# Kernel optimization log

Hardware: AMD Instinct MI355X
Metric: run time of the kernel (lower is better)

Reference implementation:

```python
import jax, jax.numpy as jnp
import numpy as np

N, H, B = 500000, 256, 512  # nodes, hidden_dim, number of graphs


def setup_inputs() -> dict:
    key = jax.random.key(0)
    k1, k2, k3, k4 = jax.random.split(key, 4)
    x = jax.random.normal(k1, (N, H), dtype=jnp.float32)
    batch = jnp.sort(jax.random.randint(k2, (N,), 0, B)).astype(jnp.int64)
    # attention_pool params (Linear(H,H) -> Tanh -> Linear(H,1))
    s1 = 1.0 / np.sqrt(H)
    W1 = jax.random.uniform(k3, (H, H), jnp.float32, -s1, s1)
    b1 = jnp.zeros((H,), jnp.float32)
    W2 = jax.random.uniform(k4, (H, 1), jnp.float32, -s1, s1)
    b2 = jnp.zeros((1,), jnp.float32)
    return {"x": x, "batch": batch, "W1": W1, "b1": b1, "W2": W2, "b2": b2}


def reference(x, batch, W1, b1, W2, b2):
    # attention scores per node: Linear -> tanh -> Linear -> scalar
    s = (jnp.tanh(x @ W1 + b1) @ W2 + b2)[:, 0]            # [N]
    # segment-wise softmax over nodes of each graph (numerically stable)
    seg_max = jax.ops.segment_max(s, batch, num_segments=B)  # [B]
    e = jnp.exp(s - seg_max[batch])                          # [N]
    denom = jax.ops.segment_sum(e, batch, num_segments=B)    # [B]
    w = e / denom[batch]                                     # [N]
    attn_pool = jax.ops.segment_sum(x * w[:, None], batch, num_segments=B)  # [B,H]
    # mean pool
    sums = jax.ops.segment_sum(x, batch, num_segments=B)     # [B,H]
    counts = jax.ops.segment_sum(jnp.ones((x.shape[0],), x.dtype), batch, num_segments=B)
    mean_pool = sums / jnp.maximum(counts, 1.0)[:, None]
    # max pool (guard empty segments -> 0, matching zero-init buffer behavior)
    max_pool = jax.ops.segment_max(x, batch, num_segments=B)
    max_pool = jnp.where(counts[:, None] > 0, max_pool, 0.0)
    return jnp.concatenate([mean_pool, max_pool, attn_pool], axis=1)  # [B, 3H]
```

## Files before the change

kernel.cpp:

```cpp
#include <hip/hip_runtime.h>

#define HDIM 256
#define MTILE 64
#define NITER 4
#define APITCH 264

typedef __attribute__((ext_vector_type(8))) short short8;
typedef __attribute__((ext_vector_type(4))) short short4v;
typedef __attribute__((ext_vector_type(4))) float floatx4;

__device__ __forceinline__ unsigned short f2bf(float f){
  unsigned u = __float_as_uint(f);
  u += 0x7FFFu + ((u>>16)&1u);
  return (unsigned short)(u>>16);
}
__device__ __forceinline__ unsigned fkey(float f){
  unsigned u = __float_as_uint(f);
  return u ^ ((unsigned)((int)u>>31) | 0x80000000u);
}
__device__ __forceinline__ float fdec(unsigned u){
  unsigned b = (u & 0x80000000u) ? (u & 0x7FFFFFFFu) : ~u;
  return __uint_as_float(b);
}

__global__ void k_pre(const float* __restrict__ W1, unsigned short* __restrict__ W1T,
                      const int* __restrict__ batch, int* __restrict__ segstart,
                      float* __restrict__ zbuf, int zerowords, int n, int B,
                      int ZB, int PB){
  const int bid = blockIdx.x, t = threadIdx.x;
  if (bid < ZB){
    int i = bid*256 + t;
    if (i < zerowords) zbuf[i] = 0.f;
  } else if (bid < ZB + PB){
    int col = bid - ZB;
    W1T[col*HDIM + t] = f2bf(W1[t*HDIM + col]);
  } else {
    int i = (bid - ZB - PB)*256 + t;
    if (i >= n) return;
    int b = batch[i];
    int prev = (i == 0) ? -1 : batch[i-1];
    if (prev != b) for (int q = prev+1; q <= b; ++q) segstart[q] = i;
    if (i == n-1) for (int q = b+1; q <= B; ++q) segstart[q] = n;
  }
}

__launch_bounds__(256)
__global__ void k_main(const float* __restrict__ x,
                       const unsigned short* __restrict__ w1t,
                       const float* __restrict__ b1,
                       const float* __restrict__ w2,
                       const float* __restrict__ b2,
                       const int* __restrict__ batch,
                       float* __restrict__ denom,
                       float* __restrict__ sums,
                       unsigned* __restrict__ maxu,
                       float* __restrict__ attn,
                       int n)
{
  __shared__ unsigned short As[MTILE*APITCH];
  __shared__ float sp[4][MTILE];
  __shared__ float earr[MTILE];
  __shared__ int sbat[MTILE*NITER];
  const int t = threadIdx.x;
  const int wv = t>>6;
  const int lane = t&63;
  const int l15 = lane&15;
  const int quad = lane>>4;
  const long long base = (long long)blockIdx.x * (MTILE*NITER);

  { long long gr = base + t; sbat[t] = (gr < n) ? batch[gr] : -1; }

  short8 bf[8][4];
  float b1v[4], w2v[4];
  const int cb = wv*64;
  #pragma unroll
  for (int ct=0; ct<4; ++ct){
    int col = cb + ct*16 + l15;
    b1v[ct] = b1[col];
    w2v[ct] = w2[col];
    #pragma unroll
    for (int kc=0; kc<8; ++kc)
      bf[kc][ct] = *(const short8*)(w1t + (size_t)col*HDIM + kc*32 + quad*8);
  }
  const float b2v = b2[0];

  float psum = 0.f, patt = 0.f, pmx = -INFINITY;
  int curb = -1;

  const float4* x4 = (const float4*)x;
  for (int it = 0; it < NITER; ++it){
    const long long node0 = base + (long long)it*MTILE;
    if (node0 >= n) break;

    #pragma unroll
    for (int j=0; j<MTILE/4; ++j){
      int f = j*256 + t;
      int row = f>>6, c4 = f&63;
      long long gr = node0 + row;
      float4 v = make_float4(0.f,0.f,0.f,0.f);
      if (gr < n) v = x4[gr*(HDIM/4) + c4];
      short4v p;
      p.x=(short)f2bf(v.x); p.y=(short)f2bf(v.y); p.z=(short)f2bf(v.z); p.w=(short)f2bf(v.w);
      *(short4v*)(As + row*APITCH + c4*4) = p;
    }
    __syncthreads();

    #pragma unroll 1
    for (int rt=0; rt<MTILE/16; ++rt){
      floatx4 acc[4];
      #pragma unroll
      for (int ct=0;ct<4;++ct) acc[ct] = (floatx4){0.f,0.f,0.f,0.f};
      #pragma unroll
      for (int kc=0; kc<8; ++kc){
        short8 a = *(const short8*)(As + (rt*16 + l15)*APITCH + kc*32 + quad*8);
        #pragma unroll
        for (int ct=0; ct<4; ++ct)
          acc[ct] = __builtin_amdgcn_mfma_f32_16x16x32_bf16(a, bf[kc][ct], acc[ct], 0, 0, 0);
      }
      float part[4] = {0.f,0.f,0.f,0.f};
      #pragma unroll
      for (int ct=0; ct<4; ++ct){
        #pragma unroll
        for (int r=0; r<4; ++r){
          float h = acc[ct][r] + b1v[ct];
          float z = fminf(fmaxf(2.f*h, -30.f), 30.f);
          float e = __expf(z);
          part[r] += __fdividef(e-1.f, e+1.f) * w2v[ct];
        }
      }
      #pragma unroll
      for (int off=8; off>=1; off>>=1){
        #pragma unroll
        for (int r=0;r<4;++r) part[r] += __shfl_xor(part[r], off, 64);
      }
      if (l15==0){
        #pragma unroll
        for (int r=0;r<4;++r) sp[wv][rt*16 + quad*4 + r] = part[r];
      }
    }
    __syncthreads();

    if (t < MTILE){
      long long gr = node0 + t;
      float e = 0.f; int b = -1;
      if (gr < n){
        float sv = sp[0][t]+sp[1][t]+sp[2][t]+sp[3][t] + b2v;
        e = __expf(sv);
        b = sbat[it*MTILE + t];
      }
      earr[t] = e;
      int b0 = __shfl(b, 0, 64);
      if (__all(b == b0)){
        float tot = e;
        #pragma unroll
        for (int off=32; off>=1; off>>=1) tot += __shfl_xor(tot, off, 64);
        if (lane==0 && b0 >= 0) atomicAdd(&denom[b0], tot);
      } else if (b >= 0){
        atomicAdd(&denom[b], e);
      }
    }
    __syncthreads();

    int rend = (int)((n - node0 < (long long)MTILE) ? (n - node0) : (long long)MTILE);
#define POOLROW(RR)                                                     \
    {                                                                   \
      int b = sbat[it*MTILE + (RR)];                                    \
      if (b != curb){                                                   \
        if (curb >= 0){                                                 \
          size_t o = (size_t)curb*HDIM + t;                             \
          atomicAdd(&sums[o], psum);                                    \
          atomicAdd(&attn[o], patt);                                    \
          atomicMax(&maxu[o], fkey(pmx));                               \
        }                                                               \
        curb = b; psum = 0.f; patt = 0.f; pmx = -INFINITY;              \
      }                                                                 \
      float v = x[(node0 + (RR))*HDIM + t];                             \
      psum += v;                                                        \
      patt = fmaf(v, earr[(RR)], patt);                                 \
      pmx = fmaxf(pmx, v);                                              \
    }
    if (rend == MTILE){
      #pragma unroll 8
      for (int r=0; r<MTILE; ++r) POOLROW(r)
    } else {
      for (int r=0; r<rend; ++r) POOLROW(r)
    }
#undef POOLROW
  }

  if (curb >= 0){
    size_t o = (size_t)curb*HDIM + t;
    atomicAdd(&sums[o], psum);
    atomicAdd(&attn[o], patt);
    atomicMax(&maxu[o], fkey(pmx));
  }
}

__global__ void k_fin(const float* __restrict__ sums, const unsigned* __restrict__ maxu,
                      const float* __restrict__ attn, const float* __restrict__ denom,
                      const int* __restrict__ segstart,
                      float* __restrict__ out, int bcount){
  int idx = blockIdx.x*256 + threadIdx.x;
  int total = bcount*3*HDIM;
  if (idx >= total) return;
  int b = idx / (3*HDIM);
  int c = idx - b*(3*HDIM);
  int cnt = segstart[b+1] - segstart[b];
  float v;
  if (c < HDIM)        v = sums[(size_t)b*HDIM + c] / fmaxf((float)cnt, 1.f);
  else if (c < 2*HDIM) v = (cnt > 0) ? fdec(maxu[(size_t)b*HDIM + (c-HDIM)]) : 0.f;
  else                 v = attn[(size_t)b*HDIM + (c-2*HDIM)] / fmaxf(denom[b], 1e-30f);
  out[idx] = v;
}

extern "C" void kernel_launch(void* const* d_in, const int* in_sizes, int n_in,
                              void* d_out, int out_size, void* d_ws, size_t ws_size,
                              hipStream_t stream){
  const float* x   = (const float*)d_in[0];
  const int* batch = (const int*)d_in[1];
  const float* W1  = (const float*)d_in[2];
  const float* b1  = (const float*)d_in[3];
  const float* W2  = (const float*)d_in[4];
  const float* b2  = (const float*)d_in[5];
  float* out = (float*)d_out;
  const int n = in_sizes[1];
  const int B = out_size / (3*HDIM);

  char* w = (char*)d_ws;
  unsigned short* W1T = (unsigned short*)w;
  size_t off = (size_t)HDIM*HDIM*2;
  int* segstart = (int*)(w + off);
  off += (size_t)((B+4)&~3)*4;
  float* stats = (float*)(w + off);
  float* denom  = stats;
  float* sums   = stats + B;
  unsigned* maxu = (unsigned*)(stats + B + (size_t)B*HDIM);
  float* attn   = stats + B + 2*(size_t)B*HDIM;
  int zerowords = B + 3*B*HDIM;

  int ZB  = (zerowords + 255)/256;
  int PB  = HDIM;
  int NBB = (n + 255)/256;
  hipLaunchKernelGGL(k_pre, dim3(ZB + PB + NBB), dim3(256), 0, stream,
                     W1, W1T, batch, segstart, stats, zerowords, n, B, ZB, PB);
  hipLaunchKernelGGL(k_main, dim3((n + MTILE*NITER - 1)/(MTILE*NITER)), dim3(256), 0, stream,
                     x, W1T, b1, W2, b2, batch, denom, sums, maxu, attn, n);
  hipLaunchKernelGGL(k_fin, dim3((out_size + 255)/256), dim3(256), 0, stream,
                     sums, maxu, attn, denom, segstart, out, B);
}
```

Baseline: 1.076 ms.

## Split pooling rows across waves with float4 lanes and drop the softmax barrier

The pooling phase is repartitioned so that each wave owns 16 rows of the tile and each lane handles 4 contiguous columns through float4 loads, instead of every thread walking all 64 rows for one column. Each wave now computes its own rows' exp scores and reduces them to the denominator with shuffles. This removes the shared earr buffer and one __syncthreads per iteration. The price is four times as many partial flushes, since each wave flushes separately and each flush issues 12 scalar atomics per lane. Segment boundaries now also appear per wave, which adds more atomic traffic on the sums, attn and maxu buffers.

```diff
diff --git a/kernel.cpp b/kernel.cpp
--- a/kernel.cpp
+++ b/kernel.cpp
@@ -59,7 +59,6 @@
 {
   __shared__ unsigned short As[MTILE*APITCH];
   __shared__ float sp[4][MTILE];
-  __shared__ float earr[MTILE];
   __shared__ int sbat[MTILE*NITER];
   const int t = threadIdx.x;
   const int wv = t>>6;
@@ -84,8 +83,32 @@
   }
   const float b2v = b2[0];
 
-  float psum = 0.f, patt = 0.f, pmx = -INFINITY;
+  float4 psum = make_float4(0.f,0.f,0.f,0.f);
+  float4 patt = make_float4(0.f,0.f,0.f,0.f);
+  float4 pmx  = make_float4(-INFINITY,-INFINITY,-INFINITY,-INFINITY);
   int curb = -1;
+  const int rb = wv*16;
+
+#define FLUSH()                                                         \
+  {                                                                     \
+    size_t o = (size_t)curb*HDIM + 4*lane;                              \
+    atomicAdd(&sums[o+0], psum.x); atomicAdd(&sums[o+1], psum.y);       \
+    atomicAdd(&sums[o+2], psum.z); atomicAdd(&sums[o+3], psum.w);       \
+    atomicAdd(&attn[o+0], patt.x); atomicAdd(&attn[o+1], patt.y);       \
+    atomicAdd(&attn[o+2], patt.z); atomicAdd(&attn[o+3], patt.w);       \
+    atomicMax(&maxu[o+0], fkey(pmx.x)); atomicMax(&maxu[o+1], fkey(pmx.y)); \
+    atomicMax(&maxu[o+2], fkey(pmx.z)); atomicMax(&maxu[o+3], fkey(pmx.w)); \
+  }
+#define ACCROW(GR, WT)                                                  \
+  {                                                                     \
+    float4 v = x4[(GR)*(HDIM/4) + lane];                                \
+    float ww = (WT);                                                    \
+    psum.x += v.x; psum.y += v.y; psum.z += v.z; psum.w += v.w;         \
+    patt.x = fmaf(v.x, ww, patt.x); patt.y = fmaf(v.y, ww, patt.y);     \
+    patt.z = fmaf(v.z, ww, patt.z); patt.w = fmaf(v.w, ww, patt.w);     \
+    pmx.x = fmaxf(pmx.x, v.x); pmx.y = fmaxf(pmx.y, v.y);               \
+    pmx.z = fmaxf(pmx.z, v.z); pmx.w = fmaxf(pmx.w, v.w);               \
+  }
 
   const float4* x4 = (const float4*)x;
   for (int it = 0; it < NITER; ++it){
@@ -140,60 +163,62 @@
     }
     __syncthreads();
 
-    if (t < MTILE){
-      long long gr = node0 + t;
-      float e = 0.f; int b = -1;
-      if (gr < n){
-        float sv = sp[0][t]+sp[1][t]+sp[2][t]+sp[3][t] + b2v;
-        e = __expf(sv);
-        b = sbat[it*MTILE + t];
-      }
-      earr[t] = e;
-      int b0 = __shfl(b, 0, 64);
-      if (__all(b == b0)){
-        float tot = e;
-        #pragma unroll
-        for (int off=32; off>=1; off>>=1) tot += __shfl_xor(tot, off, 64);
-        if (lane==0 && b0 >= 0) atomicAdd(&denom[b0], tot);
-      } else if (b >= 0){
-        atomicAdd(&denom[b], e);
-      }
-    }
-    __syncthreads();
-
-    int rend = (int)((n - node0 < (long long)MTILE) ? (n - node0) : (long long)MTILE);
-#define POOLROW(RR)                                                     \
-    {                                                                   \
-      int b = sbat[it*MTILE + (RR)];                                    \
-      if (b != curb){                                                   \
-        if (curb >= 0){                                                 \
-          size_t o = (size_t)curb*HDIM + t;                             \
-          atomicAdd(&sums[o], psum);                                    \
-          atomicAdd(&attn[o], patt);                                    \
-          atomicMax(&maxu[o], fkey(pmx));                               \
-        }                                                               \
-        curb = b; psum = 0.f; patt = 0.f; pmx = -INFINITY;              \
-      }                                                                 \
-      float v = x[(node0 + (RR))*HDIM + t];                             \
-      psum += v;                                                        \
-      patt = fmaf(v, earr[(RR)], patt);                                 \
-      pmx = fmaxf(pmx, v);                                              \
-    }
-    if (rend == MTILE){
-      #pragma unroll 8
-      for (int r=0; r<MTILE; ++r) POOLROW(r)
-    } else {
-      for (int r=0; r<rend; ++r) POOLROW(r)
-    }
-#undef POOLROW
-  }
-
-  if (curb >= 0){
-    size_t o = (size_t)curb*HDIM + t;
-    atomicAdd(&sums[o], psum);
-    atomicAdd(&attn[o], patt);
-    atomicMax(&maxu[o], fkey(pmx));
-  }
+    const int myrow = rb + l15;
+    float e_own = 0.f;
+    int b_own = sbat[it*MTILE + myrow];
+    if (node0 + myrow < n){
+      float sv = sp[0][myrow]+sp[1][myrow]+sp[2][myrow]+sp[3][myrow] + b2v;
+      e_own = __expf(sv);
+    }
+    {
+      int bfirst = __shfl(b_own, 0, 64);
+      if (__all(b_own == bfirst)){
+        float tot = e_own;
+        #pragma unroll
+        for (int off=8; off>=1; off>>=1) tot += __shfl_xor(tot, off, 64);
+        if (lane==0 && bfirst >= 0) atomicAdd(&denom[bfirst], tot);
+      } else if (lane < 16 && b_own >= 0){
+        atomicAdd(&denom[b_own], e_own);
+      }
+    }
+
+    {
+      int rend = (int)(((n - node0) < (long long)MTILE) ? (n - node0) : (long long)MTILE);
+      int whi = rb + 16 < rend ? rb + 16 : rend;
+      if (rb < rend){
+        int bhead = sbat[it*MTILE + rb];
+        int btail = sbat[it*MTILE + whi - 1];
+        if (bhead == btail && whi == rb + 16){
+          if (bhead != curb){
+            if (curb >= 0) FLUSH();
+            curb = bhead;
+            psum = make_float4(0.f,0.f,0.f,0.f);
+            patt = make_float4(0.f,0.f,0.f,0.f);
+            pmx  = make_float4(-INFINITY,-INFINITY,-INFINITY,-INFINITY);
+          }
+          #pragma unroll
+          for (int r=0; r<16; ++r)
+            ACCROW(node0 + rb + r, __shfl(e_own, r, 64))
+        } else {
+          for (int r=rb; r<whi; ++r){
+            int b = sbat[it*MTILE + r];
+            if (b != curb){
+              if (curb >= 0) FLUSH();
+              curb = b;
+              psum = make_float4(0.f,0.f,0.f,0.f);
+              patt = make_float4(0.f,0.f,0.f,0.f);
+              pmx  = make_float4(-INFINITY,-INFINITY,-INFINITY,-INFINITY);
+            }
+            ACCROW(node0 + r, __shfl(e_own, r - rb, 64))
+          }
+        }
+      }
+    }
+  }
+
+  if (curb >= 0) FLUSH();
+#undef FLUSH
+#undef ACCROW
 }
 
 __global__ void k_fin(const float* __restrict__ sums, const unsigned* __restrict__ maxu,
```

Result: no change. 1.056 ms (-1.8%).

## Split fused score+pool kernel into separate scores and chunked pooling kernels

Applied to the files above, without the earlier changes.

Splits the fused kernel into a score kernel that writes per-node exp scores to a workspace buffer and a separate pooling kernel that re-reads x and accumulates sum, max and weighted sum in register chunks of 16 rows. The pooling pass gains batched independent loads and lower register and LDS pressure. The cost is reading x a second time (about 512MB) plus an extra launch and the e buffer.

```diff
diff --git a/kernel.cpp b/kernel.cpp
--- a/kernel.cpp
+++ b/kernel.cpp
@@ -4,6 +4,8 @@
 #define MTILE 64
 #define NITER 4
 #define APITCH 264
+#define PROWS 256
+#define CHUNK 16
 
 typedef __attribute__((ext_vector_type(8))) short short8;
 typedef __attribute__((ext_vector_type(4))) short short4v;
@@ -45,30 +47,23 @@
 }
 
 __launch_bounds__(256)
-__global__ void k_main(const float* __restrict__ x,
-                       const unsigned short* __restrict__ w1t,
-                       const float* __restrict__ b1,
-                       const float* __restrict__ w2,
-                       const float* __restrict__ b2,
-                       const int* __restrict__ batch,
-                       float* __restrict__ denom,
-                       float* __restrict__ sums,
-                       unsigned* __restrict__ maxu,
-                       float* __restrict__ attn,
-                       int n)
+__global__ void k_scores(const float* __restrict__ x,
+                         const unsigned short* __restrict__ w1t,
+                         const float* __restrict__ b1,
+                         const float* __restrict__ w2,
+                         const float* __restrict__ b2,
+                         const int* __restrict__ batch,
+                         float* __restrict__ eo,
+                         float* __restrict__ denom, int n)
 {
   __shared__ unsigned short As[MTILE*APITCH];
   __shared__ float sp[4][MTILE];
-  __shared__ float earr[MTILE];
-  __shared__ int sbat[MTILE*NITER];
   const int t = threadIdx.x;
   const int wv = t>>6;
   const int lane = t&63;
   const int l15 = lane&15;
   const int quad = lane>>4;
   const long long base = (long long)blockIdx.x * (MTILE*NITER);
-
-  { long long gr = base + t; sbat[t] = (gr < n) ? batch[gr] : -1; }
 
   short8 bf[8][4];
   float b1v[4], w2v[4];
@@ -84,9 +79,6 @@
   }
   const float b2v = b2[0];
 
-  float psum = 0.f, patt = 0.f, pmx = -INFINITY;
-  int curb = -1;
-
   const float4* x4 = (const float4*)x;
   for (int it = 0; it < NITER; ++it){
     const long long node0 = base + (long long)it*MTILE;
@@ -146,9 +138,9 @@
       if (gr < n){
         float sv = sp[0][t]+sp[1][t]+sp[2][t]+sp[3][t] + b2v;
         e = __expf(sv);
-        b = sbat[it*MTILE + t];
-      }
-      earr[t] = e;
+        eo[gr] = e;
+        b = batch[gr];
+      }
       int b0 = __shfl(b, 0, 64);
       if (__all(b == b0)){
         float tot = e;
@@ -159,41 +151,51 @@
         atomicAdd(&denom[b], e);
       }
     }
-    __syncthreads();
-
-    int rend = (int)((n - node0 < (long long)MTILE) ? (n - node0) : (long long)MTILE);
-#define POOLROW(RR)                                                     \
-    {                                                                   \
-      int b = sbat[it*MTILE + (RR)];                                    \
-      if (b != curb){                                                   \
-        if (curb >= 0){                                                 \
-          size_t o = (size_t)curb*HDIM + t;                             \
-          atomicAdd(&sums[o], psum);                                    \
-          atomicAdd(&attn[o], patt);                                    \
-          atomicMax(&maxu[o], fkey(pmx));                               \
-        }                                                               \
-        curb = b; psum = 0.f; patt = 0.f; pmx = -INFINITY;              \
-      }                                                                 \
-      float v = x[(node0 + (RR))*HDIM + t];                             \
-      psum += v;                                                        \
-      patt = fmaf(v, earr[(RR)], patt);                                 \
-      pmx = fmaxf(pmx, v);                                              \
-    }
-    if (rend == MTILE){
-      #pragma unroll 8
-      for (int r=0; r<MTILE; ++r) POOLROW(r)
+  }
+}
+
+__launch_bounds__(256)
+__global__ void k_pool(const float* __restrict__ x, const int* __restrict__ batch,
+                       const float* __restrict__ e,
+                       float* __restrict__ sums, unsigned* __restrict__ maxu,
+                       float* __restrict__ attn, int n){
+  const int t = threadIdx.x;
+  long long r0 = (long long)blockIdx.x * PROWS;
+  if (r0 >= n) return;
+  long long r1 = r0 + PROWS; if (r1 > n) r1 = n;
+  int curb = batch[r0];
+  float sum=0.f, att=0.f, mx=-INFINITY;
+  long long i = r0;
+  while (i < r1){
+    if (i + CHUNK <= r1 && batch[i + CHUNK - 1] == curb){
+      float v[CHUNK], w[CHUNK];
+      #pragma unroll
+      for (int k=0;k<CHUNK;++k) v[k] = x[(i+k)*HDIM + t];
+      #pragma unroll
+      for (int k=0;k<CHUNK;++k) w[k] = e[i+k];
+      #pragma unroll
+      for (int k=0;k<CHUNK;++k){
+        sum += v[k];
+        att = fmaf(v[k], w[k], att);
+        mx = fmaxf(mx, v[k]);
+      }
+      i += CHUNK;
     } else {
-      for (int r=0; r<rend; ++r) POOLROW(r)
-    }
-#undef POOLROW
-  }
-
-  if (curb >= 0){
-    size_t o = (size_t)curb*HDIM + t;
-    atomicAdd(&sums[o], psum);
-    atomicAdd(&attn[o], patt);
-    atomicMax(&maxu[o], fkey(pmx));
-  }
+      int b = batch[i];
+      if (b != curb){
+        atomicAdd(&sums[(size_t)curb*HDIM + t], sum);
+        atomicAdd(&attn[(size_t)curb*HDIM + t], att);
+        atomicMax(&maxu[(size_t)curb*HDIM + t], fkey(mx));
+        curb=b; sum=0.f; att=0.f; mx=-INFINITY;
+      }
+      float v = x[i*HDIM + t];
+      sum += v; att = fmaf(v, e[i], att); mx = fmaxf(mx, v);
+      ++i;
+    }
+  }
+  atomicAdd(&sums[(size_t)curb*HDIM + t], sum);
+  atomicAdd(&attn[(size_t)curb*HDIM + t], att);
+  atomicMax(&maxu[(size_t)curb*HDIM + t], fkey(mx));
 }
 
 __global__ void k_fin(const float* __restrict__ sums, const unsigned* __restrict__ maxu,
@@ -229,6 +231,8 @@
   char* w = (char*)d_ws;
   unsigned short* W1T = (unsigned short*)w;
   size_t off = (size_t)HDIM*HDIM*2;
+  float* e = (float*)(w + off);
+  off += (size_t)((n+3)&~3)*4;
   int* segstart = (int*)(w + off);
   off += (size_t)((B+4)&~3)*4;
   float* stats = (float*)(w + off);
@@ -243,8 +247,10 @@
   int NBB = (n + 255)/256;
   hipLaunchKernelGGL(k_pre, dim3(ZB + PB + NBB), dim3(256), 0, stream,
                      W1, W1T, batch, segstart, stats, zerowords, n, B, ZB, PB);
-  hipLaunchKernelGGL(k_main, dim3((n + MTILE*NITER - 1)/(MTILE*NITER)), dim3(256), 0, stream,
-                     x, W1T, b1, W2, b2, batch, denom, sums, maxu, attn, n);
-  hipLaunchKernelGGL(k_fin, dim3((out_size + 255)/256), dim3(256), 0, stream,
+  hipLaunchKernelGGL(k_scores, dim3((n + MTILE*NITER - 1)/(MTILE*NITER)), dim3(256), 0, stream,
+                     x, W1T, b1, W2, b2, batch, e, denom, n);
+  hipLaunchKernelGGL(k_pool, dim3((n+PROWS-1)/PROWS), dim3(256), 0, stream,
+                     x, batch, e, sums, maxu, attn, n);
+  hipLaunchKernelGGL(k_fin, dim3((out_size+255)/256), dim3(256), 0, stream,
                      sums, maxu, attn, denom, segstart, out, B);
 }
```

Measured after the change: 906.6 us. -15.7%, faster.
